# Kernel optimization log

Hardware: AMD Instinct MI355X
Metric: run time of the kernel (lower is better)

## Reference

```python
import jax, jax.numpy as jnp
import numpy as np
import math

B, S, D, H, G = 2, 2048, 2048, 16, 4
DH = D // H          # 128 head dim
BASE = 1_000_000.0   # RoPE base


def _rope(x):
    # x: (..., S, DH); interleaved RoPE matching the torch module
    pos = jnp.arange(S, dtype=jnp.float32)[:, None]            # (S,1)
    i = jnp.arange(DH // 2, dtype=jnp.float32)                 # (DH/2,)
    omega = jnp.exp(-2.0 * i / DH * math.log(BASE))            # (DH/2,)
    ang = pos * omega                                          # (S, DH/2)
    sin = jnp.repeat(jnp.sin(ang), 2, axis=-1)                 # (S, DH)
    cos = jnp.repeat(jnp.cos(ang), 2, axis=-1)                 # (S, DH)
    xe, xo = x[..., 0::2], x[..., 1::2]
    rot = jnp.stack([-xo, xe], axis=-1).reshape(x.shape)       # (-x1,x0,-x3,x2,...)
    return x * cos + rot * sin


def setup_inputs() -> dict:
    key = jax.random.key(0)
    ks = jax.random.split(key, 5)
    x = jax.random.normal(ks[0], (B, S, D), jnp.float32)
    wq = jax.random.normal(ks[1], (D, D), jnp.float32) * 0.02
    wk = jax.random.normal(ks[2], (DH * G, D), jnp.float32) * 0.02
    wv = jax.random.normal(ks[3], (DH * G, D), jnp.float32) * 0.02
    wo = jax.random.normal(ks[4], (D, D), jnp.float32) * 0.02
    bq = jnp.zeros((D,), jnp.float32)
    bk = jnp.zeros((DH * G,), jnp.float32)
    bv = jnp.zeros((DH * G,), jnp.float32)
    bo = jnp.zeros((D,), jnp.float32)
    masked = jnp.broadcast_to(jnp.triu(jnp.ones((S, S), bool), 1), (B * H, S, S))
    return {"x": x, "wq": wq, "bq": bq, "wk": wk, "bk": bk, "wv": wv,
            "bv": bv, "wo": wo, "bo": bo, "masked": masked}


def reference(x, wq, bq, wk, bk, wv, bv, wo, bo, masked):
    r = H // G  # q heads per kv head; repeat_interleave order -> q head h uses kv h//r
    q = (x @ wq.T + bq).reshape(B, S, H, DH).transpose(0, 2, 1, 3)   # (B,H,S,DH)
    k = (x @ wk.T + bk).reshape(B, S, G, DH).transpose(0, 2, 1, 3)   # (B,G,S,DH)
    v = (x @ wv.T + bv).reshape(B, S, G, DH).transpose(0, 2, 1, 3)   # (B,G,S,DH)
    q = _rope(q)
    k = _rope(k)
    qg = q.reshape(B, G, r, S, DH)                                    # group q heads by kv head
    scores = jnp.einsum('bgrsd,bgtd->bgrst', qg, k)                   # (B,G,r,S,S)
    m = masked.reshape(B, G, r, S, S)
    scores = jnp.where(m, -jnp.inf, scores)
    attn = jax.nn.softmax(scores / math.sqrt(DH), axis=-1)
    out = jnp.einsum('bgrst,bgtd->bgrsd', attn, v)                    # (B,G,r,S,DH)
    out = out.reshape(B, H, S, DH).transpose(0, 2, 1, 3).reshape(B, S, D)
    return out @ wo.T + bo
```

## Files before the change

kernel.cpp:

```cpp
#include <hip/hip_runtime.h>

typedef unsigned short u16;
typedef __attribute__((ext_vector_type(4))) float f32x4;
typedef __attribute__((ext_vector_type(8))) __bf16 bf16x8;

static __device__ __forceinline__ u16 f2bf(float f) {
  unsigned u = __float_as_uint(f);
  u += 0x7FFFu + ((u >> 16) & 1u);
  return (u16)(u >> 16);
}
static __device__ __forceinline__ float bf2f(u16 h) {
  return __uint_as_float(((unsigned)h) << 16);
}

#define GLOAD16(gsrc, ldst)                                                    \
  __builtin_amdgcn_global_load_lds(                                            \
      (const __attribute__((address_space(1))) unsigned int*)(gsrc),           \
      (__attribute__((address_space(3))) unsigned int*)(ldst), 16, 0, 0)

__global__ void k_cvt5(const float* __restrict__ x, const float* __restrict__ wq,
                       const float* __restrict__ wk, const float* __restrict__ wv,
                       const float* __restrict__ wo, u16* __restrict__ xb,
                       u16* __restrict__ wqkvb, u16* __restrict__ wob) {
  int i = blockIdx.x * blockDim.x + threadIdx.x;
  const float* src;
  u16* dst;
  if (i < 2097152) { src = x + (size_t)i * 4; dst = xb + (size_t)i * 4; }
  else if (i < 3145728) { src = wq + (size_t)(i - 2097152) * 4; dst = wqkvb + (size_t)(i - 2097152) * 4; }
  else if (i < 3407872) { src = wk + (size_t)(i - 3145728) * 4; dst = wqkvb + (size_t)(i - 2097152) * 4; }
  else if (i < 3670016) { src = wv + (size_t)(i - 3407872) * 4; dst = wqkvb + (size_t)(i - 2097152) * 4; }
  else { src = wo + (size_t)(i - 3670016) * 4; dst = wob + (size_t)(i - 3670016) * 4; }
  float4 v = *(const float4*)src;
  ushort4 o;
  o.x = f2bf(v.x); o.y = f2bf(v.y); o.z = f2bf(v.z); o.w = f2bf(v.w);
  *(ushort4*)dst = o;
}

template <int MODE>
__global__ __launch_bounds__(256) void k_gemm_bt(const u16* __restrict__ A,
                                                 const u16* __restrict__ Bt,
                                                 const float* __restrict__ bias,
                                                 void* __restrict__ Cv,
                                                 u16* __restrict__ VtG,
                                                 int M, int N, int K) {
  __shared__ __align__(128) char smem[16384];
  const int tid = threadIdx.x;
  const int lane = tid & 63;
  const int wave = tid >> 6;
  const int m0 = blockIdx.y << 7;
  const int n0 = blockIdx.x << 7;
  const int wr = (wave >> 1) << 6;
  const int wc = (wave & 1) << 6;

  f32x4 acc[4][4];
#pragma unroll
  for (int m = 0; m < 4; ++m)
#pragma unroll
    for (int n = 0; n < 4; ++n) acc[m][n] = (f32x4){0.f, 0.f, 0.f, 0.f};

  const int nk = K >> 5;
  for (int kt = 0; kt < nk; ++kt) {
    const int kk0 = kt << 5;
#pragma unroll
    for (int iss = 0; iss < 4; ++iss) {
      int o = tid * 16 + iss * 4096;
      int lo = o & 8191;
      int row = lo >> 6;
      int cs = ((lo >> 4) & 3) ^ (row & 3);
      const u16* src =
          (o >= 8192 ? Bt + (size_t)(n0 + row) * K : A + (size_t)(m0 + row) * K) + kk0 + cs * 8;
      GLOAD16(src, smem + iss * 4096 + wave * 1024);
    }
    __syncthreads();
    bf16x8 af[4], bfr[4];
#pragma unroll
    for (int m = 0; m < 4; ++m) {
      int r = wr + m * 16 + (lane & 15);
      af[m] = *(const bf16x8*)(smem + r * 64 + (((lane >> 4) ^ (r & 3)) << 4));
    }
#pragma unroll
    for (int n = 0; n < 4; ++n) {
      int r = wc + n * 16 + (lane & 15);
      bfr[n] = *(const bf16x8*)(smem + 8192 + r * 64 + (((lane >> 4) ^ (r & 3)) << 4));
    }
#pragma unroll
    for (int m = 0; m < 4; ++m)
#pragma unroll
      for (int n = 0; n < 4; ++n)
        acc[m][n] = __builtin_amdgcn_mfma_f32_16x16x32_bf16(af[m], bfr[n], acc[m][n], 0, 0, 0);
    __syncthreads();
  }

  if (MODE == 2 && n0 >= 2560) {
#pragma unroll
    for (int n = 0; n < 4; ++n) {
      int col = n0 + wc + n * 16 + (lane & 15);
      int vd = col - 2560;
      float bsv = bias[col];
      u16* vrow = VtG + ((size_t)vd) * 2048;
#pragma unroll
      for (int m = 0; m < 4; ++m) {
        int rb = m0 + wr + m * 16 + ((lane >> 4) << 2);
        int bb = rb >> 11, ss = rb & 2047;
        ushort4 w;
        w.x = f2bf(acc[m][n][0] + bsv);
        w.y = f2bf(acc[m][n][1] + bsv);
        w.z = f2bf(acc[m][n][2] + bsv);
        w.w = f2bf(acc[m][n][3] + bsv);
        *(ushort4*)(vrow + (size_t)bb * (512 * 2048) + ss) = w;
      }
    }
    return;
  }

#pragma unroll
  for (int n = 0; n < 4; ++n) {
    int col = n0 + wc + n * 16 + (lane & 15);
    float bsv = bias[col];
#pragma unroll
    for (int m = 0; m < 4; ++m) {
      int rb = m0 + wr + m * 16 + ((lane >> 4) << 2);
#pragma unroll
      for (int j = 0; j < 4; ++j) {
        float v = acc[m][n][j] + bsv;
        if (MODE == 1)
          ((float*)Cv)[(size_t)(rb + j) * N + col] = v;
        else
          ((u16*)Cv)[(size_t)(rb + j) * N + col] = f2bf(v);
      }
    }
  }
}

__global__ void k_rope(u16* __restrict__ qkv) {
  int t = blockIdx.x * blockDim.x + threadIdx.x;
  int row = t / 1280;
  int p = t - row * 1280;
  int head = p >> 6;
  int i = p & 63;
  int s = row & 2047;
  int col = head < 16 ? (head << 7) + (i << 1) : 2048 + ((head - 16) << 7) + (i << 1);
  u16* ptr = qkv + (size_t)row * 3072 + col;
  ushort2 xv = *(ushort2*)ptr;
  float xe = bf2f(xv.x), xo = bf2f(xv.y);
  float omega = __expf(-0.21586735f * (float)i);
  float ang = (float)s * omega;
  float sn, cs;
  sincosf(ang, &sn, &cs);
  float re = xe * cs - xo * sn;
  float ro = xo * cs + xe * sn;
  if (head < 16) { re *= 0.08838834764831845f; ro *= 0.08838834764831845f; }
  ushort2 ov;
  ov.x = f2bf(re); ov.y = f2bf(ro);
  *(ushort2*)ptr = ov;
}

__global__ __launch_bounds__(256) void k_attn(const u16* __restrict__ qkv,
                                              const u16* __restrict__ vtg,
                                              u16* __restrict__ Ob) {
  __shared__ __align__(128) char smem[40960];
  const int tid = threadIdx.x, lane = tid & 63, wave = tid >> 6;
  const int g16 = lane >> 4;
  const int l15 = lane & 15;
  const int bh = blockIdx.x;
  const int Q0 = (31 - blockIdx.y) << 6;
  const int b = bh >> 4, h = bh & 15, gq = h >> 2;
  const int brow = b << 11;
  const int qcol = h << 7;
  const int kcol = 2048 + (gq << 7);
  const u16* vt_base = vtg + ((size_t)((b << 2) + gq) << 7) * 2048;

  bf16x8 qf[4];
  {
    int qrow = brow + Q0 + wave * 16 + l15;
    const u16* qp = qkv + (size_t)qrow * 3072 + qcol + (g16 << 3);
#pragma unroll
    for (int kk = 0; kk < 4; ++kk) qf[kk] = *(const bf16x8*)(qp + kk * 32);
  }

  f32x4 oacc[8];
#pragma unroll
  for (int d = 0; d < 8; ++d) oacc[d] = (f32x4){0.f, 0.f, 0.f, 0.f};
  float mrow[4], lrow[4];
#pragma unroll
  for (int j = 0; j < 4; ++j) { mrow[j] = -1e30f; lrow[j] = 0.f; }

  const int nkt = (Q0 >> 6) + 1;
  char* const pbase = smem + 32768 + wave * 2048;

  for (int kt = 0; kt < nkt; ++kt) {
    const size_t krowg = (size_t)(brow + (kt << 6));
#pragma unroll
    for (int iss = 0; iss < 4; ++iss) {
      int o = iss * 4096 + tid * 16;
      int row = o >> 8;
      int cs = ((o >> 4) & 15) ^ (row & 7);
      const u16* src = qkv + (krowg + row) * 3072 + kcol + cs * 8;
      GLOAD16(src, smem + iss * 4096 + wave * 1024);
    }
#pragma unroll
    for (int iss = 0; iss < 4; ++iss) {
      int o = iss * 4096 + tid * 16;
      int d = o >> 7;
      int cs = ((o >> 4) & 7) ^ (d & 7);
      const u16* src = vt_base + (size_t)d * 2048 + (kt << 6) + cs * 8;
      GLOAD16(src, smem + 16384 + iss * 4096 + wave * 1024);
    }
    __syncthreads();

    f32x4 sfr[4];
#pragma unroll
    for (int kc = 0; kc < 4; ++kc) {
      f32x4 s = (f32x4){0.f, 0.f, 0.f, 0.f};
      int r = kc * 16 + l15;
#pragma unroll
      for (int kk = 0; kk < 4; ++kk) {
        int byte = r * 256 + ((((kk << 2) + g16) ^ (r & 7)) << 4);
        bf16x8 kf = *(const bf16x8*)(smem + byte);
        s = __builtin_amdgcn_mfma_f32_16x16x32_bf16(qf[kk], kf, s, 0, 0, 0);
      }
      sfr[kc] = s;
    }
    const int qbase = Q0 + wave * 16 + (g16 << 2);
#pragma unroll
    for (int kc = 0; kc < 4; ++kc) {
      int kidx = (kt << 6) + kc * 16 + l15;
#pragma unroll
      for (int j = 0; j < 4; ++j)
        if (kidx > qbase + j) sfr[kc][j] = -3.0e38f;
    }
#pragma unroll
    for (int j = 0; j < 4; ++j) {
      float mx = fmaxf(fmaxf(sfr[0][j], sfr[1][j]), fmaxf(sfr[2][j], sfr[3][j]));
#pragma unroll
      for (int msk = 8; msk >= 1; msk >>= 1) mx = fmaxf(mx, __shfl_xor(mx, msk));
      float mnew = fmaxf(mrow[j], mx);
      float alpha = __expf(mrow[j] - mnew);
      const int q = (g16 << 2) + j;
      const int qkey = (q >> 1) & 7;
      float rs = 0.f;
#pragma unroll
      for (int kc = 0; kc < 4; ++kc) {
        float p = __expf(sfr[kc][j] - mnew);
        rs += p;
        int k = kc * 16 + l15;
        *(u16*)(pbase + q * 128 + (((k >> 3) ^ qkey) << 4) + ((k & 7) << 1)) = f2bf(p);
      }
#pragma unroll
      for (int msk = 8; msk >= 1; msk >>= 1) rs += __shfl_xor(rs, msk);
      lrow[j] = lrow[j] * alpha + rs;
      mrow[j] = mnew;
#pragma unroll
      for (int dt = 0; dt < 8; ++dt) oacc[dt][j] *= alpha;
    }
    asm volatile("s_waitcnt lgkmcnt(0)" ::: "memory");
    __builtin_amdgcn_sched_barrier(0);
#pragma unroll
    for (int ks = 0; ks < 2; ++ks) {
      bf16x8 pf = *(const bf16x8*)(pbase + l15 * 128 +
                                   ((((ks << 2) + g16) ^ ((l15 >> 1) & 7)) << 4));
#pragma unroll
      for (int dt = 0; dt < 8; ++dt) {
        int d = (dt << 4) + l15;
        bf16x8 vf = *(const bf16x8*)(smem + 16384 + d * 128 +
                                     ((((ks << 2) + g16) ^ (d & 7)) << 4));
        oacc[dt] = __builtin_amdgcn_mfma_f32_16x16x32_bf16(pf, vf, oacc[dt], 0, 0, 0);
      }
    }
    __syncthreads();
  }

#pragma unroll
  for (int j = 0; j < 4; ++j) {
    int q = Q0 + wave * 16 + (g16 << 2) + j;
    float inv = 1.0f / lrow[j];
    u16* op = Ob + (size_t)(brow + q) * 2048 + qcol + l15;
#pragma unroll
    for (int dt = 0; dt < 8; ++dt) op[dt * 16] = f2bf(oacc[dt][j] * inv);
  }
}

extern "C" void kernel_launch(void* const* d_in, const int* in_sizes, int n_in,
                              void* d_out, int out_size, void* d_ws, size_t ws_size,
                              hipStream_t stream) {
  const float* x  = (const float*)d_in[0];
  const float* wq = (const float*)d_in[1];
  const float* bq = (const float*)d_in[2];
  const float* wk = (const float*)d_in[3];
  const float* bk = (const float*)d_in[4];
  const float* wv = (const float*)d_in[5];
  const float* bv = (const float*)d_in[6];
  const float* wo = (const float*)d_in[7];
  const float* bo = (const float*)d_in[8];
  float* out = (float*)d_out;

  u16* wsu = (u16*)d_ws;
  u16* xb      = wsu;
  u16* wqkvb   = xb + (size_t)4096 * 2048;
  u16* wob     = wqkvb + (size_t)3072 * 2048;
  u16* qkv     = wob + (size_t)2048 * 2048;
  float* biascat = (float*)(qkv + (size_t)4096 * 3072);
  u16* vtg     = (u16*)(biascat + 3072);
  u16* Ob = xb;

  k_cvt5<<<18432, 256, 0, stream>>>(x, wq, wk, wv, wo, xb, wqkvb, wob);

  hipMemcpyAsync(biascat, bq, 2048 * sizeof(float), hipMemcpyDeviceToDevice, stream);
  hipMemcpyAsync(biascat + 2048, bk, 512 * sizeof(float), hipMemcpyDeviceToDevice, stream);
  hipMemcpyAsync(biascat + 2560, bv, 512 * sizeof(float), hipMemcpyDeviceToDevice, stream);

  k_gemm_bt<2><<<dim3(3072 / 128, 4096 / 128), 256, 0, stream>>>(
      xb, wqkvb, biascat, qkv, vtg, 4096, 3072, 2048);

  k_rope<<<(4096 * 1280) / 256, 256, 0, stream>>>(qkv);

  k_attn<<<dim3(32, 32), 256, 0, stream>>>(qkv, vtg, Ob);

  k_gemm_bt<1><<<dim3(2048 / 128, 4096 / 128), 256, 0, stream>>>(
      Ob, wob, bo, out, nullptr, 4096, 2048, 2048);
}
```

Baseline: 287.7 us.

## Fuse RoPE into QKV GEMM epilogue, fold bias copies into convert kernel

Applies the interleaved RoPE rotation and the query scale inside the QKV GEMM epilogue, fetching the pair partner with a lane shuffle and building cos/sin for the four consecutive rows from one sincos plus angle-addition identities. This removes the standalone rope kernel and its full read-modify-write pass over the Q/K buffer. The three bias hipMemcpyAsync calls are replaced by extra threads in the convert kernel. The attention kernel also raises wave priority around its MFMA sections. The angle-addition recurrence adds small fp32 rounding differences in the rotation.

```diff
diff --git a/kernel.cpp b/kernel.cpp
--- a/kernel.cpp
+++ b/kernel.cpp
@@ -20,8 +20,10 @@
 
 __global__ void k_cvt5(const float* __restrict__ x, const float* __restrict__ wq,
                        const float* __restrict__ wk, const float* __restrict__ wv,
-                       const float* __restrict__ wo, u16* __restrict__ xb,
-                       u16* __restrict__ wqkvb, u16* __restrict__ wob) {
+                       const float* __restrict__ wo, const float* __restrict__ bq,
+                       const float* __restrict__ bk, const float* __restrict__ bv,
+                       u16* __restrict__ xb, u16* __restrict__ wqkvb,
+                       u16* __restrict__ wob, float* __restrict__ biascat) {
   int i = blockIdx.x * blockDim.x + threadIdx.x;
   const float* src;
   u16* dst;
@@ -29,7 +31,15 @@
   else if (i < 3145728) { src = wq + (size_t)(i - 2097152) * 4; dst = wqkvb + (size_t)(i - 2097152) * 4; }
   else if (i < 3407872) { src = wk + (size_t)(i - 3145728) * 4; dst = wqkvb + (size_t)(i - 2097152) * 4; }
   else if (i < 3670016) { src = wv + (size_t)(i - 3407872) * 4; dst = wqkvb + (size_t)(i - 2097152) * 4; }
-  else { src = wo + (size_t)(i - 3670016) * 4; dst = wob + (size_t)(i - 3670016) * 4; }
+  else if (i < 4718592) { src = wo + (size_t)(i - 3670016) * 4; dst = wob + (size_t)(i - 3670016) * 4; }
+  else {
+    int t = i - 4718592;
+    const float* s2 = (t < 512) ? bq + t * 4
+                     : (t < 640) ? bk + (t - 512) * 4
+                                 : bv + (t - 640) * 4;
+    ((float4*)biascat)[t] = *(const float4*)s2;
+    return;
+  }
   float4 v = *(const float4*)src;
   ushort4 o;
   o.x = f2bf(v.x); o.y = f2bf(v.y); o.z = f2bf(v.z); o.w = f2bf(v.w);
@@ -113,6 +123,38 @@
     return;
   }
 
+  if (MODE == 2) {
+#pragma unroll
+    for (int n = 0; n < 4; ++n) {
+      int col = n0 + wc + n * 16 + (lane & 15);
+      float bsv = bias[col];
+      float omega = __expf(-0.21586735f * (float)((col & 127) >> 1));
+      float sd1, cd1, sd2, cd2, sd3, cd3;
+      sincosf(omega, &sd1, &cd1);
+      sincosf(omega * 2.f, &sd2, &cd2);
+      sincosf(omega * 3.f, &sd3, &cd3);
+      const bool odd = col & 1;
+      const float qsc = (col < 2048) ? 0.08838834764831845f : 1.0f;
+#pragma unroll
+      for (int m = 0; m < 4; ++m) {
+        int rb = m0 + wr + m * 16 + ((lane >> 4) << 2);
+        float s0, c0;
+        sincosf((float)(rb & 2047) * omega, &s0, &c0);
+        float css[4] = {c0, c0 * cd1 - s0 * sd1, c0 * cd2 - s0 * sd2, c0 * cd3 - s0 * sd3};
+        float snn[4] = {s0, s0 * cd1 + c0 * sd1, s0 * cd2 + c0 * sd2, s0 * cd3 + c0 * sd3};
+#pragma unroll
+        for (int j = 0; j < 4; ++j) {
+          float v = acc[m][n][j] + bsv;
+          float partner = __shfl_xor(v, 1);
+          float r = odd ? fmaf(v, css[j], partner * snn[j])
+                        : fmaf(v, css[j], -partner * snn[j]);
+          ((u16*)Cv)[(size_t)(rb + j) * N + col] = f2bf(r * qsc);
+        }
+      }
+    }
+    return;
+  }
+
 #pragma unroll
   for (int n = 0; n < 4; ++n) {
     int col = n0 + wc + n * 16 + (lane & 15);
@@ -123,36 +165,10 @@
 #pragma unroll
       for (int j = 0; j < 4; ++j) {
         float v = acc[m][n][j] + bsv;
-        if (MODE == 1)
-          ((float*)Cv)[(size_t)(rb + j) * N + col] = v;
-        else
-          ((u16*)Cv)[(size_t)(rb + j) * N + col] = f2bf(v);
-      }
-    }
-  }
-}
-
-__global__ void k_rope(u16* __restrict__ qkv) {
-  int t = blockIdx.x * blockDim.x + threadIdx.x;
-  int row = t / 1280;
-  int p = t - row * 1280;
-  int head = p >> 6;
-  int i = p & 63;
-  int s = row & 2047;
-  int col = head < 16 ? (head << 7) + (i << 1) : 2048 + ((head - 16) << 7) + (i << 1);
-  u16* ptr = qkv + (size_t)row * 3072 + col;
-  ushort2 xv = *(ushort2*)ptr;
-  float xe = bf2f(xv.x), xo = bf2f(xv.y);
-  float omega = __expf(-0.21586735f * (float)i);
-  float ang = (float)s * omega;
-  float sn, cs;
-  sincosf(ang, &sn, &cs);
-  float re = xe * cs - xo * sn;
-  float ro = xo * cs + xe * sn;
-  if (head < 16) { re *= 0.08838834764831845f; ro *= 0.08838834764831845f; }
-  ushort2 ov;
-  ov.x = f2bf(re); ov.y = f2bf(ro);
-  *(ushort2*)ptr = ov;
+        ((float*)Cv)[(size_t)(rb + j) * N + col] = v;
+      }
+    }
+  }
 }
 
 __global__ __launch_bounds__(256) void k_attn(const u16* __restrict__ qkv,
@@ -209,6 +225,7 @@
     __syncthreads();
 
     f32x4 sfr[4];
+    __builtin_amdgcn_s_setprio(1);
 #pragma unroll
     for (int kc = 0; kc < 4; ++kc) {
       f32x4 s = (f32x4){0.f, 0.f, 0.f, 0.f};
@@ -221,6 +238,7 @@
       }
       sfr[kc] = s;
     }
+    __builtin_amdgcn_s_setprio(0);
     const int qbase = Q0 + wave * 16 + (g16 << 2);
 #pragma unroll
     for (int kc = 0; kc < 4; ++kc) {
@@ -255,6 +273,7 @@
     }
     asm volatile("s_waitcnt lgkmcnt(0)" ::: "memory");
     __builtin_amdgcn_sched_barrier(0);
+    __builtin_amdgcn_s_setprio(1);
 #pragma unroll
     for (int ks = 0; ks < 2; ++ks) {
       bf16x8 pf = *(const bf16x8*)(pbase + l15 * 128 +
@@ -267,6 +286,7 @@
         oacc[dt] = __builtin_amdgcn_mfma_f32_16x16x32_bf16(pf, vf, oacc[dt], 0, 0, 0);
       }
     }
+    __builtin_amdgcn_s_setprio(0);
     __syncthreads();
   }
 
@@ -303,17 +323,12 @@
   u16* vtg     = (u16*)(biascat + 3072);
   u16* Ob = xb;
 
-  k_cvt5<<<18432, 256, 0, stream>>>(x, wq, wk, wv, wo, xb, wqkvb, wob);
-
-  hipMemcpyAsync(biascat, bq, 2048 * sizeof(float), hipMemcpyDeviceToDevice, stream);
-  hipMemcpyAsync(biascat + 2048, bk, 512 * sizeof(float), hipMemcpyDeviceToDevice, stream);
-  hipMemcpyAsync(biascat + 2560, bv, 512 * sizeof(float), hipMemcpyDeviceToDevice, stream);
+  k_cvt5<<<18435, 256, 0, stream>>>(x, wq, wk, wv, wo, bq, bk, bv,
+                                    xb, wqkvb, wob, biascat);
 
   k_gemm_bt<2><<<dim3(3072 / 128, 4096 / 128), 256, 0, stream>>>(
       xb, wqkvb, biascat, qkv, vtg, 4096, 3072, 2048);
 
-  k_rope<<<(4096 * 1280) / 256, 256, 0, stream>>>(qkv);
-
   k_attn<<<dim3(32, 32), 256, 0, stream>>>(qkv, vtg, Ob);
 
   k_gemm_bt<1><<<dim3(2048 / 128, 4096 / 128), 256, 0, stream>>>(
```

Result: faster. 264.2 us (-8.2%).
